# Kernel optimization log

Measured on AMD Instinct MI355X. Metric: run time of the kernel, lower is better.

The kernel has to match this reference:

```python
import jax, jax.numpy as jnp
import numpy as np
import math

B, S, D, H = 8, 2048, 1024, 16
DH = D // H  # attention head size = 64

def setup_inputs() -> dict:
    key = jax.random.key(0)
    ks = jax.random.split(key, 10)
    s = 1.0 / math.sqrt(D)
    return {
        "hidden_states": jax.random.normal(ks[0], (B, S, D), dtype=jnp.float32),
        "attention_mask": jnp.zeros((B, 1, S), dtype=jnp.float32),
        "Wq": jax.random.normal(ks[1], (D, D), dtype=jnp.float32) * s,
        "bq": jnp.zeros((D,), dtype=jnp.float32),
        "Wqa": jax.random.normal(ks[2], (D, H), dtype=jnp.float32) * s,
        "bqa": jnp.zeros((H,), dtype=jnp.float32),
        "Wk": jax.random.normal(ks[3], (D, D), dtype=jnp.float32) * s,
        "bk": jnp.zeros((D,), dtype=jnp.float32),
        "Wt": jax.random.normal(ks[4], (D, D), dtype=jnp.float32) * s,
        "bt": jnp.zeros((D,), dtype=jnp.float32),
    }

def reference(hidden_states, attention_mask, Wq, bq, Wqa, bqa, Wk, bk, Wt, bt):
    scale = 1.0 / math.sqrt(DH)
    q = hidden_states @ Wq + bq                      # [B,S,D] mixed_query_layer
    k = hidden_states @ Wk + bk                      # [B,S,D] mixed_key_layer
    # query attention logits -> [B,H,S]
    q_score = jnp.swapaxes(q @ Wqa + bqa, 1, 2) * scale + attention_mask
    q_weight = jax.nn.softmax(q_score, axis=-1)      # [B,H,S]
    ql = jnp.swapaxes(q.reshape(B, S, H, DH), 1, 2)  # [B,H,S,DH]
    kl = jnp.swapaxes(k.reshape(B, S, H, DH), 1, 2)  # [B,H,S,DH]
    pooled_q = jnp.einsum('bhs,bhsd->bhd', q_weight, ql)          # [B,H,DH]
    qk_score = jnp.einsum('bhsd,bhd->bhs', kl, pooled_q) * scale + attention_mask
    qk_weight = jax.nn.softmax(qk_score, axis=-1)                 # [B,H,S]
    pooled_k = jnp.einsum('bhs,bhsd->bhd', qk_weight, kl)         # [B,H,DH]
    weighted = pooled_k[:, :, None, :] * ql                       # [B,H,S,DH]
    weighted = jnp.swapaxes(weighted, 1, 2).reshape(B, S, D)      # [B,S,D]
    out = weighted @ Wt + bt + q                                  # transform + residual to query
    return out
```

## Files before the change

kernel.cpp:

```cpp
#include <hip/hip_runtime.h>
#include <hip/hip_bf16.h>
#include <math.h>

#define BB 8
#define SS 2048
#define DD 1024
#define HH 16
#define DHH 64
#define NROWS (BB*SS)
#define QSLICE ((size_t)BB * HH * SS)

typedef unsigned short u16;
typedef __attribute__((ext_vector_type(8))) __bf16 bf16x8;
typedef __attribute__((ext_vector_type(4))) float f32x4;

__device__ __forceinline__ u16 f2bf(float f) {
    union { float f; unsigned u; } v; v.f = f;
    unsigned r = v.u + 0x7fffu + ((v.u >> 16) & 1u);
    return (u16)(r >> 16);
}
__device__ __forceinline__ float bf2f(u16 b) {
    union { unsigned u; float f; } v; v.u = ((unsigned)b) << 16;
    return v.f;
}

__device__ __forceinline__ void load_lds16(const void* g, void* l) {
    __builtin_amdgcn_global_load_lds(
        (const __attribute__((address_space(1))) unsigned int*)g,
        (__attribute__((address_space(3))) unsigned int*)l,
        16, 0, 0);
}

#define BAR() do { asm volatile("" ::: "memory"); \
                   __builtin_amdgcn_s_barrier();  \
                   asm volatile("" ::: "memory"); } while (0)

__global__ __launch_bounds__(256)
void prep_kernel(const float* __restrict__ hs, u16* __restrict__ hs_bf,
                 const float* __restrict__ Wq, u16* __restrict__ WqT,
                 const float* __restrict__ Wk, u16* __restrict__ WkT,
                 const float* __restrict__ Wt, u16* __restrict__ WtT,
                 const float* __restrict__ Wqa, u16* __restrict__ WqaT,
                 float* __restrict__ pq, float* __restrict__ pk) {
    __shared__ float tile[32][33];
    const int bid = blockIdx.x;
    const int t = threadIdx.x;
    if (bid < 16384) {
        int i = bid * 256 + t;
        float4 v = ((const float4*)hs)[i];
        ushort4 o;
        o.x = f2bf(v.x); o.y = f2bf(v.y); o.z = f2bf(v.z); o.w = f2bf(v.w);
        ((ushort4*)hs_bf)[i] = o;
        return;
    }
    if (bid < 19456) {
        int rel = bid - 16384;
        const float* W; u16* WT;
        if (rel < 1024)      { W = Wq; WT = WqT; }
        else if (rel < 2048) { W = Wk; WT = WkT; rel -= 1024; }
        else                 { W = Wt; WT = WtT; rel -= 2048; }
        int m0 = (rel & 31) * 32, k0 = (rel >> 5) * 32;
        int tx = t & 31, ty = t >> 5;
        #pragma unroll
        for (int i = 0; i < 4; i++) {
            int kk = ty + i * 8;
            tile[kk][tx] = W[(k0 + kk) * DD + m0 + tx];
        }
        __syncthreads();
        #pragma unroll
        for (int i = 0; i < 4; i++) {
            int mm = ty + i * 8;
            WT[(m0 + mm) * DD + k0 + tx] = f2bf(tile[tx][mm]);
        }
        return;
    }
    if (bid < 19520) {
        int i = (bid - 19456) * 256 + t;
        int h = i >> 10, k = i & 1023;
        WqaT[i] = f2bf(Wqa[k * HH + h]);
        return;
    }
    {
        int i = (bid - 19520) * 256 + t;
        float4 z = {0.f, 0.f, 0.f, 0.f};
        if (i < 2048) ((float4*)pq)[i] = z;
        else          ((float4*)pk)[i - 2048] = z;
    }
}

template<int MODE>
__global__ __launch_bounds__(512, 2)
void gemm256_kernel(const u16* __restrict__ A, const u16* __restrict__ BT,
                    const float* __restrict__ b0, const float* __restrict__ b1,
                    const u16* __restrict__ res, float* __restrict__ Cf,
                    u16* __restrict__ C0, u16* __restrict__ C1,
                    const u16* __restrict__ WqaT, float* __restrict__ qraw) {
    __shared__ u16 smem[69632];
    const int by = blockIdx.y;
    const int row0 = blockIdx.x * 256;
    const int bcol0 = by * 256;
    const int colg0 = (MODE == 1) ? (bcol0 & 1023) : bcol0;
    const float* bias = (MODE == 1 && by >= 4) ? b1 : b0;
    u16* Cb = (MODE == 1 && by >= 4) ? C1 : C0;
    const u16* BTb = (MODE == 2) ? BT + ((size_t)(row0 >> 11) << 20) : BT;

    const int t = threadIdx.x;
    const int w = t >> 6, lane = t & 63;
    const int wm = w >> 2, wn = w & 3;
    const int m16 = lane & 15, quad = lane >> 4;

    f32x4 acc[8][4];
    #pragma unroll
    for (int i = 0; i < 8; i++)
        #pragma unroll
        for (int j = 0; j < 4; j++)
            acc[i][j] = (f32x4){0.f, 0.f, 0.f, 0.f};

    const int srow = t >> 3;
    const int scol = ((t & 7) ^ (srow & 7)) * 8;
    const u16* Ag = A + (size_t)(row0 + srow) * DD + scol;
    const u16* Bg = BTb + (size_t)(bcol0 + srow) * DD + scol;

    auto STAGE_H = [&](int ktile, int mat, int half) {
        if (ktile >= 16) return;
        const int buf = ktile & 1;
        const int k0 = ktile * 64;
        const u16* g = mat ? Bg : Ag;
        u16* s = smem + mat * 32768 + buf * 16384;
        #pragma unroll
        for (int j = 0; j < 2; ++j)
            load_lds16(g + k0 + (size_t)(half * 128 + j * 64) * DD,
                       s + half * 8192 + j * 4096 + t * 8);
    };

    STAGE_H(0, 0, 0); STAGE_H(0, 0, 1); STAGE_H(0, 1, 0); STAGE_H(0, 1, 1);
    STAGE_H(1, 0, 0);
    asm volatile("s_waitcnt vmcnt(2)" ::: "memory");
    BAR();

    for (int kt = 0; kt < 16; ++kt) {
        const int cur = kt & 1;
        const u16* sAc = smem + cur * 16384;
        const u16* sBc = smem + 32768 + cur * 16384;
        bf16x8 af[4][2], bfr[4][2];

        #pragma unroll
        for (int mi = 0; mi < 4; ++mi)
            #pragma unroll
            for (int ks = 0; ks < 2; ++ks)
                af[mi][ks] = *(const bf16x8*)&sAc[(wm * 128 + mi * 16 + m16) * 64 +
                                                 (((ks * 4 + quad) ^ (m16 & 7)) * 8)];
        #pragma unroll
        for (int ni = 0; ni < 2; ++ni)
            #pragma unroll
            for (int ks = 0; ks < 2; ++ks)
                bfr[ni][ks] = *(const bf16x8*)&sBc[(wn * 64 + ni * 16 + m16) * 64 +
                                                   (((ks * 4 + quad) ^ (m16 & 7)) * 8)];
        STAGE_H(kt + 1, 0, 1);
        BAR();
        __builtin_amdgcn_s_setprio(1);
        #pragma unroll
        for (int mi = 0; mi < 4; ++mi)
            #pragma unroll
            for (int ni = 0; ni < 2; ++ni)
                #pragma unroll
                for (int ks = 0; ks < 2; ++ks)
                    acc[mi][ni] = __builtin_amdgcn_mfma_f32_16x16x32_bf16(
                        bfr[ni][ks], af[mi][ks], acc[mi][ni], 0, 0, 0);
        __builtin_amdgcn_s_setprio(0);
        BAR();

        #pragma unroll
        for (int ni = 2; ni < 4; ++ni)
            #pragma unroll
            for (int ks = 0; ks < 2; ++ks)
                bfr[ni][ks] = *(const bf16x8*)&sBc[(wn * 64 + ni * 16 + m16) * 64 +
                                                   (((ks * 4 + quad) ^ (m16 & 7)) * 8)];
        STAGE_H(kt + 1, 1, 0);
        BAR();
        __builtin_amdgcn_s_setprio(1);
        #pragma unroll
        for (int mi = 0; mi < 4; ++mi)
            #pragma unroll
            for (int ni = 2; ni < 4; ++ni)
                #pragma unroll
                for (int ks = 0; ks < 2; ++ks)
                    acc[mi][ni] = __builtin_amdgcn_mfma_f32_16x16x32_bf16(
                        bfr[ni][ks], af[mi][ks], acc[mi][ni], 0, 0, 0);
        __builtin_amdgcn_s_setprio(0);
        BAR();

        #pragma unroll
        for (int mi = 0; mi < 4; ++mi)
            #pragma unroll
            for (int ks = 0; ks < 2; ++ks)
                af[mi][ks] = *(const bf16x8*)&sAc[(wm * 128 + (4 + mi) * 16 + m16) * 64 +
                                                 (((ks * 4 + quad) ^ (m16 & 7)) * 8)];
        STAGE_H(kt + 1, 1, 1);
        BAR();
        __builtin_amdgcn_s_setprio(1);
        #pragma unroll
        for (int mi = 0; mi < 4; ++mi)
            #pragma unroll
            for (int ni = 0; ni < 2; ++ni)
                #pragma unroll
                for (int ks = 0; ks < 2; ++ks)
                    acc[4 + mi][ni] = __builtin_amdgcn_mfma_f32_16x16x32_bf16(
                        bfr[ni][ks], af[mi][ks], acc[4 + mi][ni], 0, 0, 0);
        __builtin_amdgcn_s_setprio(0);
        BAR();

        STAGE_H(kt + 2, 0, 0);
        BAR();
        __builtin_amdgcn_s_setprio(1);
        #pragma unroll
        for (int mi = 0; mi < 4; ++mi)
            #pragma unroll
            for (int ni = 2; ni < 4; ++ni)
                #pragma unroll
                for (int ks = 0; ks < 2; ++ks)
                    acc[4 + mi][ni] = __builtin_amdgcn_mfma_f32_16x16x32_bf16(
                        bfr[ni][ks], af[mi][ks], acc[4 + mi][ni], 0, 0, 0);
        __builtin_amdgcn_s_setprio(0);
        if (kt < 14) asm volatile("s_waitcnt vmcnt(2)" ::: "memory");
        else         asm volatile("s_waitcnt vmcnt(0)" ::: "memory");
        BAR();
    }

    u16* sC = smem;
    #pragma unroll
    for (int mi = 0; mi < 8; ++mi) {
        const int lrow = wm * 128 + mi * 16 + m16;
        #pragma unroll
        for (int ni = 0; ni < 4; ++ni) {
            const int lcol = wn * 64 + ni * 16 + quad * 4;
            const float4 bv = *(const float4*)&bias[colg0 + lcol];
            if (MODE == 1) {
                ushort4 o;
                o.x = f2bf(acc[mi][ni][0] + bv.x);
                o.y = f2bf(acc[mi][ni][1] + bv.y);
                o.z = f2bf(acc[mi][ni][2] + bv.z);
                o.w = f2bf(acc[mi][ni][3] + bv.w);
                *(ushort4*)&sC[(size_t)lrow * 272 + lcol] = o;
            } else {
                const size_t idx = (size_t)(row0 + lrow) * DD + colg0 + lcol;
                const ushort4 rv = *(const ushort4*)&res[idx];
                float4 o;
                o.x = acc[mi][ni][0] + bv.x + bf2f(rv.x);
                o.y = acc[mi][ni][1] + bv.y + bf2f(rv.y);
                o.z = acc[mi][ni][2] + bv.z + bf2f(rv.z);
                o.w = acc[mi][ni][3] + bv.w + bf2f(rv.w);
                *(float4*)&Cf[idx] = o;
            }
        }
    }
    if (MODE == 1) {
        __syncthreads();
        #pragma unroll
        for (int it = 0; it < 16; ++it) {
            const int r = it * 16 + (t >> 5);
            const int c = t & 31;
            uint4 v = *(const uint4*)&sC[(size_t)r * 272 + c * 8];
            *(uint4*)&Cb[(size_t)(row0 + r) * DD + colg0 + c * 8] = v;
        }
        if (by < 4) {
            const int bIdx = row0 >> 11;
            bf16x8 wq[8];
            const u16* bp = WqaT + (size_t)m16 * DD + by * 256 + quad * 8;
            #pragma unroll
            for (int kk = 0; kk < 8; ++kk) wq[kk] = *(const bf16x8*)(bp + kk * 32);
            #pragma unroll
            for (int rt = 0; rt < 2; ++rt) {
                const int sr = (w * 2 + rt) * 16;
                f32x4 qa = (f32x4){0.f, 0.f, 0.f, 0.f};
                #pragma unroll
                for (int kk = 0; kk < 8; ++kk) {
                    bf16x8 a = *(const bf16x8*)&sC[(size_t)(sr + m16) * 272 + quad * 8 + kk * 32];
                    qa = __builtin_amdgcn_mfma_f32_16x16x32_bf16(a, wq[kk], qa, 0, 0, 0);
                }
                #pragma unroll
                for (int r = 0; r < 4; ++r) {
                    int s = (row0 & 2047) + sr + quad * 4 + r;
                    qraw[((size_t)(by * BB + bIdx) * HH + m16) * SS + s] = qa[r];
                }
            }
        }
    }
}

__global__ __launch_bounds__(256)
void wtscale_kernel(const u16* __restrict__ WtT, const float* __restrict__ pk,
                    u16* __restrict__ WtT8) {
    size_t i = (size_t)blockIdx.x * 256 + threadIdx.x;
    int b = (int)(i >> 17);
    size_t off = (i & 131071) << 3;
    int d = (int)(off & 1023);
    const float4 p0 = *(const float4*)&pk[b * 1024 + d];
    const float4 p1 = *(const float4*)&pk[b * 1024 + d + 4];
    ushort4 a0 = ((const ushort4*)(WtT + off))[0];
    ushort4 a1 = ((const ushort4*)(WtT + off))[1];
    ushort4 o0, o1;
    o0.x = f2bf(bf2f(a0.x) * p0.x); o0.y = f2bf(bf2f(a0.y) * p0.y);
    o0.z = f2bf(bf2f(a0.z) * p0.z); o0.w = f2bf(bf2f(a0.w) * p0.w);
    o1.x = f2bf(bf2f(a1.x) * p1.x); o1.y = f2bf(bf2f(a1.y) * p1.y);
    o1.z = f2bf(bf2f(a1.z) * p1.z); o1.w = f2bf(bf2f(a1.w) * p1.w);
    u16* dst = WtT8 + ((size_t)b << 20) + off;
    ((ushort4*)dst)[0] = o0;
    ((ushort4*)dst)[1] = o1;
}

template<bool EPI>
__global__ __launch_bounds__(256)
void softmax_kernel(float* __restrict__ score, const float* __restrict__ bqa,
                    const float* __restrict__ mask) {
    int bh = blockIdx.x;
    int b = bh >> 4, h = bh & 15;
    float* srow = score + ((size_t)bh << 11);
    __shared__ float rm[4], rs[4];
    int t = threadIdx.x;

    float v[8];
    float m = -1e30f;
    #pragma unroll
    for (int i = 0; i < 8; i++) {
        int off = t + i * 256;
        float x;
        if (EPI) {
            x = srow[off] + srow[off + QSLICE] + srow[off + 2 * QSLICE] + srow[off + 3 * QSLICE];
            x = (x + bqa[h]) * 0.125f + mask[b * SS + off];
        } else {
            x = srow[off];
        }
        v[i] = x; m = fmaxf(m, x);
    }
    #pragma unroll
    for (int off = 32; off; off >>= 1) m = fmaxf(m, __shfl_xor(m, off));
    if ((t & 63) == 0) rm[t >> 6] = m;
    __syncthreads();
    m = fmaxf(fmaxf(rm[0], rm[1]), fmaxf(rm[2], rm[3]));

    float sum = 0.f;
    #pragma unroll
    for (int i = 0; i < 8; i++) { v[i] = __expf(v[i] - m); sum += v[i]; }
    #pragma unroll
    for (int off = 32; off; off >>= 1) sum += __shfl_xor(sum, off);
    if ((t & 63) == 0) rs[t >> 6] = sum;
    __syncthreads();
    float inv = 1.0f / (rs[0] + rs[1] + rs[2] + rs[3]);
    #pragma unroll
    for (int i = 0; i < 8; i++) srow[t + i * 256] = v[i] * inv;
}

__global__ __launch_bounds__(256)
void pool_kernel(const float* __restrict__ w, const u16* __restrict__ X,
                 float* __restrict__ pooled) {
    int b = blockIdx.x;
    int s0 = blockIdx.y * 32;
    int t = threadIdx.x;
    int wid = t >> 6, lane = t & 63;
    int h = lane >> 2;
    __shared__ float sw[16 * 33];
    __shared__ float pr[4][64 * 17];
    {
        int hh = t >> 4, si = t & 15;
        const float* wr = w + ((size_t)(b * HH + hh) << 11) + s0;
        sw[hh * 33 + si] = wr[si];
        sw[hh * 33 + si + 16] = wr[si + 16];
    }
    __syncthreads();
    float acc[16];
    #pragma unroll
    for (int j = 0; j < 16; j++) acc[j] = 0.f;
    const u16* xbase = X + ((size_t)(b * SS + s0 + wid * 8) << 10) + lane * 16;
    #pragma unroll
    for (int rr = 0; rr < 8; rr++) {
        float ws = sw[h * 33 + wid * 8 + rr];
        const uint4* xp = (const uint4*)(xbase + (size_t)rr * DD);
        uint4 x0 = xp[0], x1 = xp[1];
        unsigned xw[8] = {x0.x, x0.y, x0.z, x0.w, x1.x, x1.y, x1.z, x1.w};
        #pragma unroll
        for (int i2 = 0; i2 < 8; i2++) {
            union { unsigned u; float f; } lo, hi;
            lo.u = xw[i2] << 16; hi.u = xw[i2] & 0xffff0000u;
            acc[2 * i2]     += ws * lo.f;
            acc[2 * i2 + 1] += ws * hi.f;
        }
    }
    #pragma unroll
    for (int j = 0; j < 16; j++) pr[wid][lane * 17 + j] = acc[j];
    __syncthreads();
    #pragma unroll
    for (int i = 0; i < 4; i++) {
        int idx = t + i * 256;
        int l2 = idx >> 4, j2 = idx & 15;
        float v = pr[0][l2 * 17 + j2] + pr[1][l2 * 17 + j2] +
                  pr[2][l2 * 17 + j2] + pr[3][l2 * 17 + j2];
        int od = (l2 >> 2) * 64 + (l2 & 3) * 16 + j2;
        atomicAdd(&pooled[b * DD + od], v);
    }
}

__global__ __launch_bounds__(256)
void qkscore_kernel(const u16* __restrict__ kbf, const float* __restrict__ pq,
                    const float* __restrict__ mask, float* __restrict__ qkscore) {
    int row = blockIdx.x * 4 + (threadIdx.x >> 6);
    int lane = threadIdx.x & 63;
    int b = row >> 11, s = row & 2047;
    int h = lane >> 2, dp = lane & 3;
    const u16* kp = kbf + (size_t)row * DD + h * 64 + dp * 16;
    const float* pqp = pq + (size_t)(b * HH + h) * 64 + dp * 16;
    const uint4* kp4 = (const uint4*)kp;
    uint4 ka = kp4[0], kb4 = kp4[1];
    unsigned kw[8] = {ka.x, ka.y, ka.z, ka.w, kb4.x, kb4.y, kb4.z, kb4.w};
    float acc = 0.f;
    #pragma unroll
    for (int i = 0; i < 8; i++) {
        union { unsigned u; float f; } lo, hi;
        lo.u = kw[i] << 16;
        hi.u = kw[i] & 0xffff0000u;
        acc += lo.f * pqp[2 * i] + hi.f * pqp[2 * i + 1];
    }
    acc += __shfl_xor(acc, 1);
    acc += __shfl_xor(acc, 2);
    if (dp == 0) qkscore[(size_t)(b * HH + h) * SS + s] = acc * 0.125f + mask[b * SS + s];
}

extern "C" void kernel_launch(void* const* d_in, const int* in_sizes, int n_in,
                              void* d_out, int out_size, void* d_ws, size_t ws_size,
                              hipStream_t stream) {
    const float* hs   = (const float*)d_in[0];
    const float* mask = (const float*)d_in[1];
    const float* Wq   = (const float*)d_in[2];
    const float* bq   = (const float*)d_in[3];
    const float* Wqa  = (const float*)d_in[4];
    const float* bqa  = (const float*)d_in[5];
    const float* Wk   = (const float*)d_in[6];
    const float* bk   = (const float*)d_in[7];
    const float* Wt   = (const float*)d_in[8];
    const float* bt   = (const float*)d_in[9];
    float* out = (float*)d_out;

    char* ws = (char*)d_ws;
    u16*   hs_bf = (u16*)ws;   ws += (size_t)NROWS * DD * 2;
    u16*   WqT   = (u16*)ws;   ws += (size_t)DD * DD * 2;
    u16*   WkT   = (u16*)ws;   ws += (size_t)DD * DD * 2;
    u16*   WtT   = (u16*)ws;   ws += (size_t)DD * DD * 2;
    u16*   WqaT  = (u16*)ws;   ws += (size_t)HH * DD * 2;
    u16*   q_bf  = (u16*)ws;   ws += (size_t)NROWS * DD * 2;
    u16*   k_bf  = (u16*)ws;   ws += (size_t)NROWS * DD * 2;
    float* qraw  = (float*)ws; ws += QSLICE * 4 * 4;
    float* qksc  = (float*)ws; ws += (size_t)BB * HH * SS * 4;
    float* pq    = (float*)ws; ws += (size_t)BB * HH * 64 * 4;
    float* pk    = (float*)ws; ws += (size_t)BB * HH * 64 * 4;
    u16*   WtT8  = hs_bf;

    prep_kernel<<<19536, 256, 0, stream>>>(hs, hs_bf, Wq, WqT, Wk, WkT, Wt, WtT,
                                           Wqa, WqaT, pq, pk);

    gemm256_kernel<1><<<dim3(NROWS / 256, 8), 512, 0, stream>>>(
        hs_bf, WqT, bq, bk, nullptr, nullptr, q_bf, k_bf, WqaT, qraw);

    softmax_kernel<true><<<BB * HH, 256, 0, stream>>>(qraw, bqa, mask);
    pool_kernel<<<dim3(BB, SS / 32), 256, 0, stream>>>(qraw, q_bf, pq);
    qkscore_kernel<<<NROWS / 4, 256, 0, stream>>>(k_bf, pq, mask, qksc);
    softmax_kernel<false><<<BB * HH, 256, 0, stream>>>(qksc, nullptr, nullptr);
    pool_kernel<<<dim3(BB, SS / 32), 256, 0, stream>>>(qksc, k_bf, pk);
    wtscale_kernel<<<4096, 256, 0, stream>>>(WtT, pk, WtT8);

    gemm256_kernel<2><<<dim3(NROWS / 256, 4), 512, 0, stream>>>(
        q_bf, WtT8, bt, nullptr, q_bf, out, nullptr, nullptr, nullptr, nullptr);
}
```

Baseline: 287.4 us.

## Fuse softmax, pooling and qk-score stages into one per-head kernel

Replaces five launches (two softmaxes, two pooling kernels with atomics, and the qk-score kernel) with a single kernel that runs one block per (batch, head). Each block keeps the softmax weights and pooled query in shared memory, which removes the intermediate score buffers, the atomic accumulation and the zero-init of pq/pk. The cost is that only 128 blocks process the whole middle stage, so parallelism drops and each block reads 2048 rows of strided 128-byte head slices from q and k twice.

Measured after the change: 285.1 us. Within noise of the previous version (-0.8%).

```diff
diff --git a/kernel.cpp b/kernel.cpp
--- a/kernel.cpp
+++ b/kernel.cpp
@@ -40,8 +40,7 @@
                  const float* __restrict__ Wq, u16* __restrict__ WqT,
                  const float* __restrict__ Wk, u16* __restrict__ WkT,
                  const float* __restrict__ Wt, u16* __restrict__ WtT,
-                 const float* __restrict__ Wqa, u16* __restrict__ WqaT,
-                 float* __restrict__ pq, float* __restrict__ pk) {
+                 const float* __restrict__ Wqa, u16* __restrict__ WqaT) {
     __shared__ float tile[32][33];
     const int bid = blockIdx.x;
     const int t = threadIdx.x;
@@ -74,17 +73,10 @@
         }
         return;
     }
-    if (bid < 19520) {
+    {
         int i = (bid - 19456) * 256 + t;
         int h = i >> 10, k = i & 1023;
         WqaT[i] = f2bf(Wqa[k * HH + h]);
-        return;
-    }
-    {
-        int i = (bid - 19520) * 256 + t;
-        float4 z = {0.f, 0.f, 0.f, 0.f};
-        if (i < 2048) ((float4*)pq)[i] = z;
-        else          ((float4*)pk)[i - 2048] = z;
     }
 }
 
@@ -288,6 +280,151 @@
     }
 }
 
+__global__ __launch_bounds__(512)
+void attnmid_kernel(const float* __restrict__ qraw, const float* __restrict__ bqa,
+                    const float* __restrict__ mask, const u16* __restrict__ qbf,
+                    const u16* __restrict__ kbf, float* __restrict__ pk) {
+    const int bh = blockIdx.x;
+    const int b = bh >> 4, h = bh & 15;
+    const int t = threadIdx.x;
+    const int wid = t >> 6, lane = t & 63;
+    __shared__ float sw[SS];
+    __shared__ float red[8];
+    __shared__ float prr[8][64];
+    __shared__ float pql[64];
+
+    {
+        const float* qr = qraw + ((size_t)bh << 11);
+        float v[4]; float m = -1e30f;
+        #pragma unroll
+        for (int i = 0; i < 4; i++) {
+            int off = t + i * 512;
+            float x = qr[off] + qr[off + QSLICE] + qr[off + 2 * QSLICE] + qr[off + 3 * QSLICE];
+            x = (x + bqa[h]) * 0.125f + mask[b * SS + off];
+            v[i] = x; m = fmaxf(m, x);
+        }
+        #pragma unroll
+        for (int o = 32; o; o >>= 1) m = fmaxf(m, __shfl_xor(m, o));
+        if (lane == 0) red[wid] = m;
+        __syncthreads();
+        m = red[0];
+        #pragma unroll
+        for (int i = 1; i < 8; i++) m = fmaxf(m, red[i]);
+        float sum = 0.f;
+        #pragma unroll
+        for (int i = 0; i < 4; i++) { v[i] = __expf(v[i] - m); sum += v[i]; }
+        #pragma unroll
+        for (int o = 32; o; o >>= 1) sum += __shfl_xor(sum, o);
+        __syncthreads();
+        if (lane == 0) red[wid] = sum;
+        __syncthreads();
+        float tot = 0.f;
+        #pragma unroll
+        for (int i = 0; i < 8; i++) tot += red[i];
+        float inv = 1.0f / tot;
+        #pragma unroll
+        for (int i = 0; i < 4; i++) sw[t + i * 512] = v[i] * inv;
+        __syncthreads();
+    }
+
+    {
+        const int d0 = (lane & 31) * 2;
+        const int srel = lane >> 5;
+        const u16* base = qbf + (((size_t)b * SS) << 10) + h * 64 + d0;
+        float a0 = 0.f, a1 = 0.f;
+        #pragma unroll 8
+        for (int it = 0; it < 128; ++it) {
+            int s = wid * 256 + it * 2 + srel;
+            unsigned kw = *(const unsigned*)(base + ((size_t)s << 10));
+            float wf = sw[s];
+            union { unsigned u; float f; } lo, hi;
+            lo.u = kw << 16; hi.u = kw & 0xffff0000u;
+            a0 += wf * lo.f; a1 += wf * hi.f;
+        }
+        a0 += __shfl_xor(a0, 32); a1 += __shfl_xor(a1, 32);
+        if (lane < 32) { prr[wid][d0] = a0; prr[wid][d0 + 1] = a1; }
+        __syncthreads();
+        if (t < 64) {
+            float s2 = 0.f;
+            #pragma unroll
+            for (int w2 = 0; w2 < 8; w2++) s2 += prr[w2][t];
+            pql[t] = s2;
+        }
+        __syncthreads();
+    }
+
+    {
+        float v[4]; float m = -1e30f;
+        #pragma unroll
+        for (int i = 0; i < 4; i++) {
+            int s = t + i * 512;
+            const uint4* kp = (const uint4*)(kbf + (((size_t)(b * SS + s)) << 10) + h * 64);
+            float acc = 0.f;
+            #pragma unroll
+            for (int j = 0; j < 8; j++) {
+                uint4 kv = kp[j];
+                unsigned ww[4] = {kv.x, kv.y, kv.z, kv.w};
+                #pragma unroll
+                for (int q2 = 0; q2 < 4; q2++) {
+                    union { unsigned u; float f; } lo, hi;
+                    lo.u = ww[q2] << 16; hi.u = ww[q2] & 0xffff0000u;
+                    acc += lo.f * pql[j * 8 + q2 * 2] + hi.f * pql[j * 8 + q2 * 2 + 1];
+                }
+            }
+            float x = acc * 0.125f + mask[b * SS + s];
+            v[i] = x; m = fmaxf(m, x);
+        }
+        #pragma unroll
+        for (int o = 32; o; o >>= 1) m = fmaxf(m, __shfl_xor(m, o));
+        __syncthreads();
+        if (lane == 0) red[wid] = m;
+        __syncthreads();
+        m = red[0];
+        #pragma unroll
+        for (int i = 1; i < 8; i++) m = fmaxf(m, red[i]);
+        float sum = 0.f;
+        #pragma unroll
+        for (int i = 0; i < 4; i++) { v[i] = __expf(v[i] - m); sum += v[i]; }
+        #pragma unroll
+        for (int o = 32; o; o >>= 1) sum += __shfl_xor(sum, o);
+        __syncthreads();
+        if (lane == 0) red[wid] = sum;
+        __syncthreads();
+        float tot = 0.f;
+        #pragma unroll
+        for (int i = 0; i < 8; i++) tot += red[i];
+        float inv = 1.0f / tot;
+        #pragma unroll
+        for (int i = 0; i < 4; i++) sw[t + i * 512] = v[i] * inv;
+        __syncthreads();
+    }
+
+    {
+        const int d0 = (lane & 31) * 2;
+        const int srel = lane >> 5;
+        const u16* base = kbf + (((size_t)b * SS) << 10) + h * 64 + d0;
+        float a0 = 0.f, a1 = 0.f;
+        #pragma unroll 8
+        for (int it = 0; it < 128; ++it) {
+            int s = wid * 256 + it * 2 + srel;
+            unsigned kw = *(const unsigned*)(base + ((size_t)s << 10));
+            float wf = sw[s];
+            union { unsigned u; float f; } lo, hi;
+            lo.u = kw << 16; hi.u = kw & 0xffff0000u;
+            a0 += wf * lo.f; a1 += wf * hi.f;
+        }
+        a0 += __shfl_xor(a0, 32); a1 += __shfl_xor(a1, 32);
+        if (lane < 32) { prr[wid][d0] = a0; prr[wid][d0 + 1] = a1; }
+        __syncthreads();
+        if (t < 64) {
+            float s2 = 0.f;
+            #pragma unroll
+            for (int w2 = 0; w2 < 8; w2++) s2 += prr[w2][t];
+            pk[b * DD + h * 64 + t] = s2;
+        }
+    }
+}
+
 __global__ __launch_bounds__(256)
 void wtscale_kernel(const u16* __restrict__ WtT, const float* __restrict__ pk,
                     u16* __restrict__ WtT8) {
@@ -309,122 +446,6 @@
     ((ushort4*)dst)[1] = o1;
 }
 
-template<bool EPI>
-__global__ __launch_bounds__(256)
-void softmax_kernel(float* __restrict__ score, const float* __restrict__ bqa,
-                    const float* __restrict__ mask) {
-    int bh = blockIdx.x;
-    int b = bh >> 4, h = bh & 15;
-    float* srow = score + ((size_t)bh << 11);
-    __shared__ float rm[4], rs[4];
-    int t = threadIdx.x;
-
-    float v[8];
-    float m = -1e30f;
-    #pragma unroll
-    for (int i = 0; i < 8; i++) {
-        int off = t + i * 256;
-        float x;
-        if (EPI) {
-            x = srow[off] + srow[off + QSLICE] + srow[off + 2 * QSLICE] + srow[off + 3 * QSLICE];
-            x = (x + bqa[h]) * 0.125f + mask[b * SS + off];
-        } else {
-            x = srow[off];
-        }
-        v[i] = x; m = fmaxf(m, x);
-    }
-    #pragma unroll
-    for (int off = 32; off; off >>= 1) m = fmaxf(m, __shfl_xor(m, off));
-    if ((t & 63) == 0) rm[t >> 6] = m;
-    __syncthreads();
-    m = fmaxf(fmaxf(rm[0], rm[1]), fmaxf(rm[2], rm[3]));
-
-    float sum = 0.f;
-    #pragma unroll
-    for (int i = 0; i < 8; i++) { v[i] = __expf(v[i] - m); sum += v[i]; }
-    #pragma unroll
-    for (int off = 32; off; off >>= 1) sum += __shfl_xor(sum, off);
-    if ((t & 63) == 0) rs[t >> 6] = sum;
-    __syncthreads();
-    float inv = 1.0f / (rs[0] + rs[1] + rs[2] + rs[3]);
-    #pragma unroll
-    for (int i = 0; i < 8; i++) srow[t + i * 256] = v[i] * inv;
-}
-
-__global__ __launch_bounds__(256)
-void pool_kernel(const float* __restrict__ w, const u16* __restrict__ X,
-                 float* __restrict__ pooled) {
-    int b = blockIdx.x;
-    int s0 = blockIdx.y * 32;
-    int t = threadIdx.x;
-    int wid = t >> 6, lane = t & 63;
-    int h = lane >> 2;
-    __shared__ float sw[16 * 33];
-    __shared__ float pr[4][64 * 17];
-    {
-        int hh = t >> 4, si = t & 15;
-        const float* wr = w + ((size_t)(b * HH + hh) << 11) + s0;
-        sw[hh * 33 + si] = wr[si];
-        sw[hh * 33 + si + 16] = wr[si + 16];
-    }
-    __syncthreads();
-    float acc[16];
-    #pragma unroll
-    for (int j = 0; j < 16; j++) acc[j] = 0.f;
-    const u16* xbase = X + ((size_t)(b * SS + s0 + wid * 8) << 10) + lane * 16;
-    #pragma unroll
-    for (int rr = 0; rr < 8; rr++) {
-        float ws = sw[h * 33 + wid * 8 + rr];
-        const uint4* xp = (const uint4*)(xbase + (size_t)rr * DD);
-        uint4 x0 = xp[0], x1 = xp[1];
-        unsigned xw[8] = {x0.x, x0.y, x0.z, x0.w, x1.x, x1.y, x1.z, x1.w};
-        #pragma unroll
-        for (int i2 = 0; i2 < 8; i2++) {
-            union { unsigned u; float f; } lo, hi;
-            lo.u = xw[i2] << 16; hi.u = xw[i2] & 0xffff0000u;
-            acc[2 * i2]     += ws * lo.f;
-            acc[2 * i2 + 1] += ws * hi.f;
-        }
-    }
-    #pragma unroll
-    for (int j = 0; j < 16; j++) pr[wid][lane * 17 + j] = acc[j];
-    __syncthreads();
-    #pragma unroll
-    for (int i = 0; i < 4; i++) {
-        int idx = t + i * 256;
-        int l2 = idx >> 4, j2 = idx & 15;
-        float v = pr[0][l2 * 17 + j2] + pr[1][l2 * 17 + j2] +
-                  pr[2][l2 * 17 + j2] + pr[3][l2 * 17 + j2];
-        int od = (l2 >> 2) * 64 + (l2 & 3) * 16 + j2;
-        atomicAdd(&pooled[b * DD + od], v);
-    }
-}
-
-__global__ __launch_bounds__(256)
-void qkscore_kernel(const u16* __restrict__ kbf, const float* __restrict__ pq,
-                    const float* __restrict__ mask, float* __restrict__ qkscore) {
-    int row = blockIdx.x * 4 + (threadIdx.x >> 6);
-    int lane = threadIdx.x & 63;
-    int b = row >> 11, s = row & 2047;
-    int h = lane >> 2, dp = lane & 3;
-    const u16* kp = kbf + (size_t)row * DD + h * 64 + dp * 16;
-    const float* pqp = pq + (size_t)(b * HH + h) * 64 + dp * 16;
-    const uint4* kp4 = (const uint4*)kp;
-    uint4 ka = kp4[0], kb4 = kp4[1];
-    unsigned kw[8] = {ka.x, ka.y, ka.z, ka.w, kb4.x, kb4.y, kb4.z, kb4.w};
-    float acc = 0.f;
-    #pragma unroll
-    for (int i = 0; i < 8; i++) {
-        union { unsigned u; float f; } lo, hi;
-        lo.u = kw[i] << 16;
-        hi.u = kw[i] & 0xffff0000u;
-        acc += lo.f * pqp[2 * i] + hi.f * pqp[2 * i + 1];
-    }
-    acc += __shfl_xor(acc, 1);
-    acc += __shfl_xor(acc, 2);
-    if (dp == 0) qkscore[(size_t)(b * HH + h) * SS + s] = acc * 0.125f + mask[b * SS + s];
-}
-
 extern "C" void kernel_launch(void* const* d_in, const int* in_sizes, int n_in,
                               void* d_out, int out_size, void* d_ws, size_t ws_size,
                               hipStream_t stream) {
@@ -449,22 +470,17 @@
     u16*   q_bf  = (u16*)ws;   ws += (size_t)NROWS * DD * 2;
     u16*   k_bf  = (u16*)ws;   ws += (size_t)NROWS * DD * 2;
     float* qraw  = (float*)ws; ws += QSLICE * 4 * 4;
-    float* qksc  = (float*)ws; ws += (size_t)BB * HH * SS * 4;
-    float* pq    = (float*)ws; ws += (size_t)BB * HH * 64 * 4;
     float* pk    = (float*)ws; ws += (size_t)BB * HH * 64 * 4;
     u16*   WtT8  = hs_bf;
 
-    prep_kernel<<<19536, 256, 0, stream>>>(hs, hs_bf, Wq, WqT, Wk, WkT, Wt, WtT,
-                                           Wqa, WqaT, pq, pk);
+    prep_kernel<<<19520, 256, 0, stream>>>(hs, hs_bf, Wq, WqT, Wk, WkT, Wt, WtT,
+                                           Wqa, WqaT);
 
     gemm256_kernel<1><<<dim3(NROWS / 256, 8), 512, 0, stream>>>(
         hs_bf, WqT, bq, bk, nullptr, nullptr, q_bf, k_bf, WqaT, qraw);
 
-    softmax_kernel<true><<<BB * HH, 256, 0, stream>>>(qraw, bqa, mask);
-    pool_kernel<<<dim3(BB, SS / 32), 256, 0, stream>>>(qraw, q_bf, pq);
-    qkscore_kernel<<<NROWS / 4, 256, 0, stream>>>(k_bf, pq, mask, qksc);
-    softmax_kernel<false><<<BB * HH, 256, 0, stream>>>(qksc, nullptr, nullptr);
-    pool_kernel<<<dim3(BB, SS / 32), 256, 0, stream>>>(qksc, k_bf, pk);
+    attnmid_kernel<<<BB * HH, 512, 0, stream>>>(qraw, bqa, mask, q_bf, k_bf, pk);
+
     wtscale_kernel<<<4096, 256, 0, stream>>>(WtT, pk, WtT8);
 
     gemm256_kernel<2><<<dim3(NROWS / 256, 4), 512, 0, stream>>>(
```
